# Optimization experiments

Hardware: AMD Instinct MI355X
Metric: run time of the kernel (lower is better)

The kernel has to match this reference:

```python
import jax, jax.numpy as jnp
import numpy as np

HEAD_DIM = 32  # fixed by the module's reshape(b, d/32, 32)


def setup_inputs() -> dict:
    key = jax.random.key(0)
    kx, kw = jax.random.split(key)
    b, d = 32, 65536  # seq_len = d // 32 = 2048
    x = jax.random.normal(kx, (b, d), dtype=jnp.float32)
    # kernel: nn.init.uniform_(-0.05, 0.05), shape (3, output_dim, output_dim)
    kernel = jax.random.uniform(kw, (3, HEAD_DIM, HEAD_DIM), dtype=jnp.float32,
                                minval=-0.05, maxval=0.05)
    return {"x": x, "kernel": kernel}


def reference(x, kernel):
    b, d = x.shape
    s = d // HEAD_DIM
    xr = x.reshape(b, s, HEAD_DIM)                      # [b, s, 32]
    q = jnp.einsum('bsd,de->bse', xr, kernel[0])
    k = jnp.einsum('bsd,de->bse', xr, kernel[1])
    v = jnp.einsum('bsd,de->bse', xr, kernel[2])
    scores = jnp.einsum('bsd,btd->bst', q, k) / jnp.sqrt(jnp.float32(HEAD_DIM))
    attn = jax.nn.softmax(scores, axis=-1)              # [b, s, s]
    out = jnp.einsum('bst,btd->bsd', attn, v)           # [b, s, 32]
    return out.reshape(b, d)
```

## Files before the change

### kernel.cpp

```cpp
#include <hip/hip_runtime.h>
#include <hip/hip_bf16.h>


typedef __attribute__((ext_vector_type(8))) short bf16x8;
typedef __attribute__((ext_vector_type(4))) short bf16x4;
typedef __attribute__((ext_vector_type(4))) float f32x4;
typedef __attribute__((ext_vector_type(2))) unsigned int u32x2;
typedef __attribute__((ext_vector_type(4))) unsigned int u32x4;

#if __has_builtin(__builtin_amdgcn_mfma_f32_16x16x16bf16_1k)
#define MFMA_PV(a, b, c) __builtin_amdgcn_mfma_f32_16x16x16bf16_1k(a, b, c, 0, 0, 0)
#elif defined(__HIP_DEVICE_COMPILE__)
#error "no 16x16x16 bf16 mfma builtin on device"
#else
#define MFMA_PV(a, b, c) (c)
#endif

__device__ __forceinline__ unsigned cvt_pk_bf16(float lo, float hi) {
  unsigned r;
  asm("v_cvt_pk_bf16_f32 %0, %1, %2" : "=v"(r) : "v"(lo), "v"(hi));
  return r;
}
__device__ __forceinline__ bf16x4 as_bf16x4(u32x2 u) {
  union { u32x2 a; bf16x4 b; } c; c.a = u; return c.b;
}

__global__ __launch_bounds__(256) void qkv_kernel(
    const float* __restrict__ x, const float* __restrict__ w,
    unsigned short* __restrict__ Qb, unsigned short* __restrict__ KF,
    unsigned short* __restrict__ VP) {
  __shared__ float Wlds[3072];
  __shared__ float xs[2304];
  __shared__ __align__(16) unsigned char RP[4096];
  int tid = threadIdx.x;
  int B = blockIdx.x;

  const float* xg = x + (size_t)B * 2048;
#pragma unroll
  for (int k2 = 0; k2 < 2; ++k2) {
    int fi = k2 * 1024 + tid * 4;
    f32x4 v = *(const f32x4*)(xg + fi);
    *(f32x4*)(&xs[(fi >> 5) * 36 + (fi & 31)]) = v;
  }
#pragma unroll
  for (int i = 0; i < 12; ++i) Wlds[i * 256 + tid] = w[i * 256 + tid];
  __syncthreads();

  int L64 = tid >> 2, q = tid & 3;
  int kt = L64 >> 4, n = L64 & 15;
  int g4 = (L64 >> 2) & 3, i4 = L64 & 3;

  const float* xr = &xs[L64 * 36];
  f32x4 xv[8];
#pragma unroll
  for (int j = 0; j < 8; ++j) xv[j] = *(const f32x4*)(xr + j * 4);

  f32x4 aq0 = (f32x4)0.0f, aq1 = (f32x4)0.0f;
  f32x4 ak0 = (f32x4)0.0f, ak1 = (f32x4)0.0f;
  f32x4 av0 = (f32x4)0.0f, av1 = (f32x4)0.0f;
#pragma unroll
  for (int d = 0; d < 32; ++d) {
    float xd = xv[d >> 2][d & 3];
    const f32x4* w0 = (const f32x4*)&Wlds[d * 32 + q * 8];
    const f32x4* w1 = (const f32x4*)&Wlds[1024 + d * 32 + q * 8];
    const f32x4* w2 = (const f32x4*)&Wlds[2048 + d * 32 + q * 8];
    aq0 += xd * w0[0]; aq1 += xd * w0[1];
    ak0 += xd * w1[0]; ak1 += xd * w1[1];
    av0 += xd * w2[0]; av1 += xd * w2[1];
  }

  const float alpha = 1.4426950408889634f * 0.17677669529663687f;

  {
    u32x4 oq;
    oq[0] = cvt_pk_bf16(aq0[0] * alpha, aq0[1] * alpha);
    oq[1] = cvt_pk_bf16(aq0[2] * alpha, aq0[3] * alpha);
    oq[2] = cvt_pk_bf16(aq1[0] * alpha, aq1[1] * alpha);
    oq[3] = cvt_pk_bf16(aq1[2] * alpha, aq1[3] * alpha);
    *(u32x4*)(Qb + (size_t)(B * 64 + L64) * 32 + q * 8) = oq;
  }

  {
    u32x4 ok;
    ok[0] = cvt_pk_bf16(ak0[0], ak0[1]);
    ok[1] = cvt_pk_bf16(ak0[2], ak0[3]);
    ok[2] = cvt_pk_bf16(ak1[0], ak1[1]);
    ok[3] = cvt_pk_bf16(ak1[2], ak1[3]);
    *(u32x4*)(RP + kt * 1024 + q * 256 + n * 16) = ok;
  }
  __syncthreads();
  *(u32x4*)((char*)KF + (size_t)B * 4096 + tid * 16) = *(const u32x4*)(RP + tid * 16);
  __syncthreads();

  {
    unsigned short* Vl = (unsigned short*)RP;
    int sbase = (q >> 1) * 1024 + (kt >> 1) * 512 + g4 * 128 + (kt & 1) * 4 + i4;
#pragma unroll
    for (int oo = 0; oo < 8; ++oo) {
      float vv = (oo < 4) ? av0[oo] : av1[oo - 4];
      unsigned r = cvt_pk_bf16(vv, vv);
      int e = q * 8 + oo;
      Vl[sbase + (e & 15) * 8] = (unsigned short)(r & 0xffffu);
    }
  }
  __syncthreads();
  *(u32x4*)((char*)VP + (size_t)B * 4096 + tid * 16) = *(const u32x4*)(RP + tid * 16);
}

#define SMAX(SF, I2) {                                           \
    float p0 = __builtin_amdgcn_exp2f(SF[0]);                    \
    float p1 = __builtin_amdgcn_exp2f(SF[1]);                    \
    float p2 = __builtin_amdgcn_exp2f(SF[2]);                    \
    float p3 = __builtin_amdgcn_exp2f(SF[3]);                    \
    lsum += (p0 + p1) + (p2 + p3);                               \
    pk[I2] = cvt_pk_bf16(p0, p1);                                \
    pk[I2 + 1] = cvt_pk_bf16(p2, p3); }

#define PVKT(KT, V0, V1, ACC0, ACC1) {                           \
    u32x2 bw; bw[0] = pk[2 * KT]; bw[1] = pk[2 * KT + 1];        \
    bf16x4 bb = as_bf16x4(bw);                                   \
    ACC0 = MFMA_PV(as_bf16x4(V0), bb, ACC0);                     \
    ACC1 = MFMA_PV(as_bf16x4(V1), bb, ACC1); }

__global__ __launch_bounds__(256, 4) void attn_kernel(
    const unsigned short* __restrict__ Qb, const unsigned short* __restrict__ KF,
    const unsigned short* __restrict__ VP, float* __restrict__ out) {
  __shared__ __align__(16) unsigned char lds[2][8192];
  unsigned char* ldsb = &lds[0][0];
  int tid = threadIdx.x;
  int wv = tid >> 6, lane = tid & 63;
  int n = lane & 15, g = lane >> 4;

  int bid = blockIdx.x;
  int swz = (bid & 7) * 128 + (bid >> 3);
  int bi = swz >> 5, qt = swz & 31;

  size_t Rq = (size_t)bi * 2048 + qt * 64 + wv * 16;

  const unsigned char* Kg = (const unsigned char*)KF + (size_t)bi * 131072;
  const unsigned char* Vg = (const unsigned char*)VP + (size_t)bi * 131072;

  const unsigned char* sgp = (wv < 2 ? Kg : Vg) + (wv & 1) * 2048 + lane * 16;
  unsigned char* ldsw = ldsb + (wv < 2 ? 0 : 4096) + (wv & 1) * 2048 + lane * 16;

  bf16x8 qf = *(const bf16x8*)(Qb + (Rq + n) * 32 + g * 8);

  f32x4 oA0 = (f32x4)0.0f, oA1 = (f32x4)0.0f;
  f32x4 oB0 = (f32x4)0.0f, oB1 = (f32x4)0.0f;
  float lsum = 0.0f;

  bf16x8 kr0, kr1;

  kr0 = *(const bf16x8*)(sgp);
  kr1 = *(const bf16x8*)(sgp + 1024);
  sgp += 4096;
  *(bf16x8*)(ldsw) = kr0;
  *(bf16x8*)(ldsw + 1024) = kr1;
  __syncthreads();

  for (int t = 0; t < 32; ++t) {
    int buf = t & 1;
    if (t < 31) {
      kr0 = *(const bf16x8*)(sgp);
      kr1 = *(const bf16x8*)(sgp + 1024);
      sgp += 4096;
    }
    const unsigned char* Lp = ldsb + buf * 8192;
    bf16x8 kf0 = *(const bf16x8*)(Lp + lane * 16);
    bf16x8 kf1 = *(const bf16x8*)(Lp + lane * 16 + 1024);
    bf16x8 kf2 = *(const bf16x8*)(Lp + lane * 16 + 2048);
    bf16x8 kf3 = *(const bf16x8*)(Lp + lane * 16 + 3072);
    u32x4 w00 = *(const u32x4*)(Lp + 4096 + lane * 16);
    u32x4 w01 = *(const u32x4*)(Lp + 4096 + lane * 16 + 1024);
    u32x4 w10 = *(const u32x4*)(Lp + 4096 + lane * 16 + 2048);
    u32x4 w11 = *(const u32x4*)(Lp + 4096 + lane * 16 + 3072);
    u32x2 vf0; vf0[0] = w00[0]; vf0[1] = w00[1];
    u32x2 vf1; vf1[0] = w00[2]; vf1[1] = w00[3];
    u32x2 vf2; vf2[0] = w01[0]; vf2[1] = w01[1];
    u32x2 vf3; vf3[0] = w01[2]; vf3[1] = w01[3];
    u32x2 vf4; vf4[0] = w10[0]; vf4[1] = w10[1];
    u32x2 vf5; vf5[0] = w10[2]; vf5[1] = w10[3];
    u32x2 vf6; vf6[0] = w11[0]; vf6[1] = w11[1];
    u32x2 vf7; vf7[0] = w11[2]; vf7[1] = w11[3];
    f32x4 s0 = __builtin_amdgcn_mfma_f32_16x16x32_bf16(kf0, qf, (f32x4)0.0f, 0, 0, 0);
    f32x4 s1 = __builtin_amdgcn_mfma_f32_16x16x32_bf16(kf1, qf, (f32x4)0.0f, 0, 0, 0);
    f32x4 s2 = __builtin_amdgcn_mfma_f32_16x16x32_bf16(kf2, qf, (f32x4)0.0f, 0, 0, 0);
    f32x4 s3 = __builtin_amdgcn_mfma_f32_16x16x32_bf16(kf3, qf, (f32x4)0.0f, 0, 0, 0);
    unsigned pk[8];
    SMAX(s0, 0) SMAX(s1, 2) SMAX(s2, 4) SMAX(s3, 6)
    PVKT(0, vf0, vf4, oA0, oA1) PVKT(1, vf1, vf5, oA0, oA1)
    PVKT(2, vf2, vf6, oB0, oB1) PVKT(3, vf3, vf7, oB0, oB1)
    __syncthreads();
    if (t < 31) {
      unsigned char* Wp = ldsw + (buf ^ 1) * 8192;
      *(bf16x8*)(Wp) = kr0;
      *(bf16x8*)(Wp + 1024) = kr1;
      __syncthreads();
    }
  }

  lsum += __shfl_xor(lsum, 16);
  lsum += __shfl_xor(lsum, 32);
  float inv = 1.0f / lsum;

  f32x4 r0 = (oA0 + oB0) * inv;
  f32x4 r1 = (oA1 + oB1) * inv;
  float* ob = out + (Rq + n) * 32 + g * 4;
  *(f32x4*)(ob)      = r0;
  *(f32x4*)(ob + 16) = r1;
}

extern "C" void kernel_launch(void* const* d_in, const int* in_sizes, int n_in,
                              void* d_out, int out_size, void* d_ws, size_t ws_size,
                              hipStream_t stream) {
  const float* x = (const float*)d_in[0];
  const float* w = (const float*)d_in[1];
  float* out = (float*)d_out;

  unsigned short* KF = (unsigned short*)d_ws;
  unsigned short* VP = KF + (size_t)65536 * 32;
  unsigned short* Qb = VP + (size_t)65536 * 32;

  qkv_kernel<<<1024, 256, 0, stream>>>(x, w, Qb, KF, VP);
  attn_kernel<<<1024, 256, 0, stream>>>(Qb, KF, VP, out);
}
```

Before: 48.97 us.

## Compute QKV projection with bf16 MFMA and stage all outputs through LDS

The QKV projection moves from scalar FP32 FMAs over an LDS-staged x tile to bf16 16x16x32 MFMA instructions, with weight fragments built per lane from LDS and x loaded straight from global memory. Q, K and V are written into separate LDS regions, and all three are stored to global memory in coalesced 16-byte chunks behind a single barrier. This is meant to cut the projection's ALU cost and its extra barriers. In exchange, x and the weights are rounded to bf16 before the matmul, which adds error to the projection.

New measurement: 43.70 us. 10.8% less time.

```diff
diff --git a/kernel.cpp b/kernel.cpp
--- a/kernel.cpp
+++ b/kernel.cpp
@@ -24,87 +24,90 @@
 __device__ __forceinline__ bf16x4 as_bf16x4(u32x2 u) {
   union { u32x2 a; bf16x4 b; } c; c.a = u; return c.b;
 }
+__device__ __forceinline__ bf16x8 as_bf16x8(u32x4 u) {
+  union { u32x4 a; bf16x8 b; } c; c.a = u; return c.b;
+}
 
 __global__ __launch_bounds__(256) void qkv_kernel(
     const float* __restrict__ x, const float* __restrict__ w,
     unsigned short* __restrict__ Qb, unsigned short* __restrict__ KF,
     unsigned short* __restrict__ VP) {
   __shared__ float Wlds[3072];
-  __shared__ float xs[2304];
-  __shared__ __align__(16) unsigned char RP[4096];
+  __shared__ __align__(16) unsigned char RP[12288];
   int tid = threadIdx.x;
   int B = blockIdx.x;
-
-  const float* xg = x + (size_t)B * 2048;
-#pragma unroll
-  for (int k2 = 0; k2 < 2; ++k2) {
-    int fi = k2 * 1024 + tid * 4;
-    f32x4 v = *(const f32x4*)(xg + fi);
-    *(f32x4*)(&xs[(fi >> 5) * 36 + (fi & 31)]) = v;
-  }
+  int wv = tid >> 6, lane = tid & 63;
+  int n = lane & 15, g = lane >> 4;
+
 #pragma unroll
   for (int i = 0; i < 12; ++i) Wlds[i * 256 + tid] = w[i * 256 + tid];
   __syncthreads();
 
-  int L64 = tid >> 2, q = tid & 3;
-  int kt = L64 >> 4, n = L64 & 15;
-  int g4 = (L64 >> 2) & 3, i4 = L64 & 3;
-
-  const float* xr = &xs[L64 * 36];
-  f32x4 xv[8];
-#pragma unroll
-  for (int j = 0; j < 8; ++j) xv[j] = *(const f32x4*)(xr + j * 4);
-
-  f32x4 aq0 = (f32x4)0.0f, aq1 = (f32x4)0.0f;
-  f32x4 ak0 = (f32x4)0.0f, ak1 = (f32x4)0.0f;
-  f32x4 av0 = (f32x4)0.0f, av1 = (f32x4)0.0f;
-#pragma unroll
-  for (int d = 0; d < 32; ++d) {
-    float xd = xv[d >> 2][d & 3];
-    const f32x4* w0 = (const f32x4*)&Wlds[d * 32 + q * 8];
-    const f32x4* w1 = (const f32x4*)&Wlds[1024 + d * 32 + q * 8];
-    const f32x4* w2 = (const f32x4*)&Wlds[2048 + d * 32 + q * 8];
-    aq0 += xd * w0[0]; aq1 += xd * w0[1];
-    ak0 += xd * w1[0]; ak1 += xd * w1[1];
-    av0 += xd * w2[0]; av1 += xd * w2[1];
-  }
-
   const float alpha = 1.4426950408889634f * 0.17677669529663687f;
 
+  bf16x8 af[3][2];
+#pragma unroll
+  for (int h = 0; h < 3; ++h) {
+#pragma unroll
+    for (int jh = 0; jh < 2; ++jh) {
+      float sc = (h == 0) ? alpha : 1.0f;
+      u32x4 u;
+#pragma unroll
+      for (int p = 0; p < 4; ++p) {
+        float lo = Wlds[h * 1024 + (g * 8 + 2 * p) * 32 + jh * 16 + n] * sc;
+        float hi = Wlds[h * 1024 + (g * 8 + 2 * p + 1) * 32 + jh * 16 + n] * sc;
+        u[p] = cvt_pk_bf16(lo, hi);
+      }
+      af[h][jh] = as_bf16x8(u);
+    }
+  }
+
+  int row = B * 64 + wv * 16 + n;
+  const float* xp = x + (size_t)row * 32 + g * 8;
+  f32x4 x0 = *(const f32x4*)(xp);
+  f32x4 x1 = *(const f32x4*)(xp + 4);
+  u32x4 ux;
+  ux[0] = cvt_pk_bf16(x0[0], x0[1]);
+  ux[1] = cvt_pk_bf16(x0[2], x0[3]);
+  ux[2] = cvt_pk_bf16(x1[0], x1[1]);
+  ux[3] = cvt_pk_bf16(x1[2], x1[3]);
+  bf16x8 xf = as_bf16x8(ux);
+
+#pragma unroll
+  for (int jh = 0; jh < 2; ++jh) {
+    f32x4 d = __builtin_amdgcn_mfma_f32_16x16x32_bf16(af[0][jh], xf, (f32x4)0.0f, 0, 0, 0);
+    u32x2 o;
+    o[0] = cvt_pk_bf16(d[0], d[1]);
+    o[1] = cvt_pk_bf16(d[2], d[3]);
+    *(u32x2*)(RP + wv * 1024 + n * 64 + (jh * 16 + g * 4) * 2) = o;
+  }
+#pragma unroll
+  for (int jh = 0; jh < 2; ++jh) {
+    f32x4 d = __builtin_amdgcn_mfma_f32_16x16x32_bf16(af[1][jh], xf, (f32x4)0.0f, 0, 0, 0);
+    u32x2 o;
+    o[0] = cvt_pk_bf16(d[0], d[1]);
+    o[1] = cvt_pk_bf16(d[2], d[3]);
+    *(u32x2*)(RP + 4096 + wv * 1024 + (jh * 2 + (g >> 1)) * 256 + n * 16 + (g & 1) * 8) = o;
+  }
   {
-    u32x4 oq;
-    oq[0] = cvt_pk_bf16(aq0[0] * alpha, aq0[1] * alpha);
-    oq[1] = cvt_pk_bf16(aq0[2] * alpha, aq0[3] * alpha);
-    oq[2] = cvt_pk_bf16(aq1[0] * alpha, aq1[1] * alpha);
-    oq[3] = cvt_pk_bf16(aq1[2] * alpha, aq1[3] * alpha);
-    *(u32x4*)(Qb + (size_t)(B * 64 + L64) * 32 + q * 8) = oq;
-  }
-
-  {
-    u32x4 ok;
-    ok[0] = cvt_pk_bf16(ak0[0], ak0[1]);
-    ok[1] = cvt_pk_bf16(ak0[2], ak0[3]);
-    ok[2] = cvt_pk_bf16(ak1[0], ak1[1]);
-    ok[3] = cvt_pk_bf16(ak1[2], ak1[3]);
-    *(u32x4*)(RP + kt * 1024 + q * 256 + n * 16) = ok;
+    unsigned short* Vl = (unsigned short*)(RP + 8192);
+    int sb = (wv >> 1) * 512 + (n >> 2) * 128 + (wv & 1) * 4 + (n & 3);
+#pragma unroll
+    for (int jh = 0; jh < 2; ++jh) {
+      f32x4 d = __builtin_amdgcn_mfma_f32_16x16x32_bf16(af[2][jh], xf, (f32x4)0.0f, 0, 0, 0);
+#pragma unroll
+      for (int t = 0; t < 4; ++t) {
+        int e = jh * 16 + g * 4 + t;
+        unsigned r = cvt_pk_bf16(d[t], d[t]);
+        Vl[sb + (e >> 4) * 1024 + (e & 15) * 8] = (unsigned short)(r & 0xffffu);
+      }
+    }
   }
   __syncthreads();
-  *(u32x4*)((char*)KF + (size_t)B * 4096 + tid * 16) = *(const u32x4*)(RP + tid * 16);
-  __syncthreads();
-
-  {
-    unsigned short* Vl = (unsigned short*)RP;
-    int sbase = (q >> 1) * 1024 + (kt >> 1) * 512 + g4 * 128 + (kt & 1) * 4 + i4;
-#pragma unroll
-    for (int oo = 0; oo < 8; ++oo) {
-      float vv = (oo < 4) ? av0[oo] : av1[oo - 4];
-      unsigned r = cvt_pk_bf16(vv, vv);
-      int e = q * 8 + oo;
-      Vl[sbase + (e & 15) * 8] = (unsigned short)(r & 0xffffu);
-    }
-  }
-  __syncthreads();
-  *(u32x4*)((char*)VP + (size_t)B * 4096 + tid * 16) = *(const u32x4*)(RP + tid * 16);
+
+  *(u32x4*)((char*)Qb + (size_t)B * 4096 + tid * 16) = *(const u32x4*)(RP + tid * 16);
+  *(u32x4*)((char*)KF + (size_t)B * 4096 + tid * 16) = *(const u32x4*)(RP + 4096 + tid * 16);
+  *(u32x4*)((char*)VP + (size_t)B * 4096 + tid * 16) = *(const u32x4*)(RP + 8192 + tid * 16);
 }
 
 #define SMAX(SF, I2) {                                           \
```
